# Kernel optimization log

Hardware: AMD Instinct MI355X
Metric: run time of the kernel (lower is better)

The kernel has to match this reference:

```python
import jax, jax.numpy as jnp
import numpy as np

N = 50000
E = 800000
D_IN = 128
D_HID = 128
D_OUT = 64


def setup_inputs() -> dict:
    key = jax.random.key(0)
    ks = jax.random.split(key, 9)
    x = jax.random.normal(ks[0], (N, D_IN), dtype=jnp.float32)
    edge_index = jax.random.randint(ks[1], (2, E), 0, N, dtype=jnp.int64)
    # PyG SAGEConv params: lin_l (neighbor path, with bias), lin_r (root path, no bias)
    s1 = 1.0 / np.sqrt(D_IN)
    s2 = 1.0 / np.sqrt(D_HID)
    return {
        "x": x,
        "edge_index": edge_index,
        "W1l": jax.random.uniform(ks[2], (D_IN, D_HID), jnp.float32, -s1, s1),
        "b1": jax.random.uniform(ks[3], (D_HID,), jnp.float32, -s1, s1),
        "W1r": jax.random.uniform(ks[4], (D_IN, D_HID), jnp.float32, -s1, s1),
        "W2l": jax.random.uniform(ks[5], (D_HID, D_OUT), jnp.float32, -s2, s2),
        "b2": jax.random.uniform(ks[6], (D_OUT,), jnp.float32, -s2, s2),
        "W2r": jax.random.uniform(ks[7], (D_HID, D_OUT), jnp.float32, -s2, s2),
    }


def _sage_conv(h, src, dst, Wl, b, Wr, n_nodes):
    # mean-aggregate source features onto target nodes
    msg = h[src]  # [E, d] gather
    summed = jax.ops.segment_sum(msg, dst, num_segments=n_nodes)
    cnt = jax.ops.segment_sum(jnp.ones((src.shape[0],), h.dtype), dst, num_segments=n_nodes)
    mean = summed / jnp.maximum(cnt, 1.0)[:, None]
    return mean @ Wl + b + h @ Wr


def reference(x, edge_index, W1l, b1, W1r, W2l, b2, W2r):
    src, dst = edge_index[0], edge_index[1]
    n = x.shape[0]
    h = jax.nn.relu(_sage_conv(x, src, dst, W1l, b1, W1r, n))
    # dropout is identity in eval mode
    return _sage_conv(h, src, dst, W2l, b2, W2r, n)
```

## Files before the change

kernel.cpp:

```cpp
#include <hip/hip_runtime.h>

#define NN   50000
#define NE   800000
#define CAP  48
#define NPG  6250
#define EPB  3125
#define SEG  576

#define BIN_BLOCKS  256
#define CVT_BLOCKS  (3125 + 128)
#define ZERO_BLOCKS 196
#define SCAT_BLOCKS 2048

typedef __attribute__((ext_vector_type(8))) short bf16x8;
typedef __attribute__((ext_vector_type(4))) float f32x4;

__device__ __forceinline__ unsigned short f2b(float f) {
    unsigned int u = __builtin_bit_cast(unsigned int, f);
    u += 0x7FFFu + ((u >> 16) & 1u);
    return (unsigned short)(u >> 16);
}
__device__ __forceinline__ float b2f_lo(unsigned int u) {
    return __builtin_bit_cast(float, u << 16);
}
__device__ __forceinline__ float b2f_hi(unsigned int u) {
    return __builtin_bit_cast(float, u & 0xFFFF0000u);
}

__global__ __launch_bounds__(256) void prep_kernel(const int* __restrict__ src,
                                                   const int* __restrict__ dst,
                                                   int* __restrict__ bcnt,
                                                   unsigned* __restrict__ stage,
                                                   const float* __restrict__ x,
                                                   const float* __restrict__ W1l,
                                                   const float* __restrict__ W1r,
                                                   const float* __restrict__ W2l,
                                                   const float* __restrict__ W2r,
                                                   unsigned short* __restrict__ xb,
                                                   unsigned short* __restrict__ Bt1,
                                                   unsigned short* __restrict__ Bt2,
                                                   int* __restrict__ cursor) {
    if (blockIdx.x < BIN_BLOCKS) {
        __shared__ int cnt[16][8];
        __shared__ int repoff[16][8];
        const int tid = threadIdx.x;
        const int b   = blockIdx.x;
        const int r   = tid >> 4;
        if (tid < 128) ((int*)cnt)[tid] = 0;
        __syncthreads();

        unsigned recs[13], metas[13];
#pragma unroll
        for (int it = 0; it < 13; ++it) {
            const int i = it * 256 + tid;
            metas[it] = 0xFFFFFFFFu;
            if (i < EPB) {
                const int e = b * EPB + i;
                const int s = src[e], d = dst[e];
                const int g = d / NPG;
                const int dloc = d - g * NPG;
                const int slot = atomicAdd(&cnt[r][g], 1);
                recs[it]  = ((unsigned)dloc << 16) | (unsigned)s;
                metas[it] = ((unsigned)r << 20) | ((unsigned)g << 16) | (unsigned)slot;
            }
        }
        __syncthreads();
        if (tid < 8) {
            int off = 0;
#pragma unroll
            for (int rr = 0; rr < 16; ++rr) { repoff[rr][tid] = off; off += cnt[rr][tid]; }
            bcnt[tid * 256 + b] = off;
        }
        __syncthreads();
#pragma unroll
        for (int it = 0; it < 13; ++it) {
            if (metas[it] != 0xFFFFFFFFu) {
                const int rr   = metas[it] >> 20;
                const int g    = (metas[it] >> 16) & 7;
                const int slot = metas[it] & 0xFFFF;
                const int pos  = repoff[rr][g] + slot;
                if (pos < SEG) stage[((g << 8) + b) * SEG + pos] = recs[it];
            }
        }
    } else if (blockIdx.x < BIN_BLOCKS + 3125) {
        int i = (blockIdx.x - BIN_BLOCKS) * 256 + threadIdx.x;
        const float4* p = reinterpret_cast<const float4*>(x) + (size_t)i * 2;
        float4 a = p[0], b = p[1];
        uint4 u;
        u.x = (unsigned)f2b(a.x) | ((unsigned)f2b(a.y) << 16);
        u.y = (unsigned)f2b(a.z) | ((unsigned)f2b(a.w) << 16);
        u.z = (unsigned)f2b(b.x) | ((unsigned)f2b(b.y) << 16);
        u.w = (unsigned)f2b(b.z) | ((unsigned)f2b(b.w) << 16);
        reinterpret_cast<uint4*>(xb)[i] = u;
    } else if (blockIdx.x < BIN_BLOCKS + CVT_BLOCKS) {
        int t = (blockIdx.x - BIN_BLOCKS - 3125) * 256 + threadIdx.x;
        if (t < 32768) {
            int c = t >> 8, k = t & 255;
            float v = (k < 128) ? W1l[k * 128 + c] : W1r[(k - 128) * 128 + c];
            Bt1[c * 256 + k] = f2b(v);
        }
        if (t < 16384) {
            int c = t >> 7, k = t & 127;
            float v = (c < 64) ? W2l[k * 64 + c] : W2r[k * 64 + (c - 64)];
            Bt2[c * 128 + k] = f2b(v);
        }
    } else {
        int i = (blockIdx.x - BIN_BLOCKS - CVT_BLOCKS) * 256 + threadIdx.x;
        if (i < NN) cursor[i] = 0;
    }
}

__global__ __launch_bounds__(256) void scatter_kernel(const int* __restrict__ bcnt,
                                                      const unsigned* __restrict__ stage,
                                                      int* __restrict__ cursor,
                                                      int* __restrict__ col) {
    const int g = blockIdx.x & 7;
    const int b = blockIdx.x >> 3;
    int cnt = bcnt[g * 256 + b];
    if (cnt > SEG) cnt = SEG;
    const unsigned* sp = stage + (size_t)((g << 8) + b) * SEG;
    const int n0 = g * NPG;
    for (int i = threadIdx.x; i < cnt; i += 256) {
        unsigned rec = sp[i];
        int d = n0 + (int)(rec >> 16);
        int p = atomicAdd(&cursor[d], 1);
        if (p < CAP) col[d * CAP + p] = (int)(rec & 0xFFFFu);
    }
}

__global__ __launch_bounds__(256) void agg_gemm12(const unsigned short* __restrict__ xb,
                                                  const int* __restrict__ cursor,
                                                  const int* __restrict__ col,
                                                  const unsigned short* __restrict__ Bt1,
                                                  const unsigned short* __restrict__ Bt2,
                                                  const float* __restrict__ b1,
                                                  const float* __restrict__ b2,
                                                  unsigned short* __restrict__ hlb,
                                                  float* __restrict__ outp) {
    constexpr int LDA = 264;
    constexpr int LDH = 136;
    __shared__ unsigned short As[64 * LDA];

    const int base = blockIdx.x * 64;
    const int tid  = threadIdx.x;
    const int l    = tid & 15;
    const int sub  = tid >> 4;

    const uint4* fp = reinterpret_cast<const uint4*>(xb);

    for (int gq = 0; gq < 4; ++gq) {
        const int r  = gq * 16 + sub;
        const int gn = base + r;
        float a0 = 0.f, a1 = 0.f, a2 = 0.f, a3 = 0.f,
              a4 = 0.f, a5 = 0.f, a6 = 0.f, a7 = 0.f;
        uint4 xrow = make_uint4(0, 0, 0, 0);
        if (gn < NN) {
            int len = cursor[gn];
            len = (len > CAP) ? CAP : len;
            const int4* cp = reinterpret_cast<const int4*>(col + gn * CAP);
            int j = 0;
            for (; j + 4 <= len; j += 4) {
                int4 c4 = cp[j >> 2];
                uint4 v0 = fp[c4.x * 16 + l];
                uint4 v1 = fp[c4.y * 16 + l];
                uint4 v2 = fp[c4.z * 16 + l];
                uint4 v3 = fp[c4.w * 16 + l];
                a0 += (b2f_lo(v0.x) + b2f_lo(v1.x)) + (b2f_lo(v2.x) + b2f_lo(v3.x));
                a1 += (b2f_hi(v0.x) + b2f_hi(v1.x)) + (b2f_hi(v2.x) + b2f_hi(v3.x));
                a2 += (b2f_lo(v0.y) + b2f_lo(v1.y)) + (b2f_lo(v2.y) + b2f_lo(v3.y));
                a3 += (b2f_hi(v0.y) + b2f_hi(v1.y)) + (b2f_hi(v2.y) + b2f_hi(v3.y));
                a4 += (b2f_lo(v0.z) + b2f_lo(v1.z)) + (b2f_lo(v2.z) + b2f_lo(v3.z));
                a5 += (b2f_hi(v0.z) + b2f_hi(v1.z)) + (b2f_hi(v2.z) + b2f_hi(v3.z));
                a6 += (b2f_lo(v0.w) + b2f_lo(v1.w)) + (b2f_lo(v2.w) + b2f_lo(v3.w));
                a7 += (b2f_hi(v0.w) + b2f_hi(v1.w)) + (b2f_hi(v2.w) + b2f_hi(v3.w));
            }
            for (; j < len; ++j) {
                uint4 v0 = fp[col[gn * CAP + j] * 16 + l];
                a0 += b2f_lo(v0.x);  a1 += b2f_hi(v0.x);
                a2 += b2f_lo(v0.y);  a3 += b2f_hi(v0.y);
                a4 += b2f_lo(v0.z);  a5 += b2f_hi(v0.z);
                a6 += b2f_lo(v0.w);  a7 += b2f_hi(v0.w);
            }
            const float inv = 1.0f / fmaxf((float)len, 1.0f);
            a0 *= inv; a1 *= inv; a2 *= inv; a3 *= inv;
            a4 *= inv; a5 *= inv; a6 *= inv; a7 *= inv;
            xrow = fp[gn * 16 + l];
        }
        uint4 u;
        u.x = (unsigned)f2b(a0) | ((unsigned)f2b(a1) << 16);
        u.y = (unsigned)f2b(a2) | ((unsigned)f2b(a3) << 16);
        u.z = (unsigned)f2b(a4) | ((unsigned)f2b(a5) << 16);
        u.w = (unsigned)f2b(a6) | ((unsigned)f2b(a7) << 16);
        *reinterpret_cast<uint4*>(&As[r * LDA + l * 8])       = u;
        *reinterpret_cast<uint4*>(&As[r * LDA + 128 + l * 8]) = xrow;
    }
    __syncthreads();

    const int wid  = tid >> 6, lane = tid & 63;
    const int lr   = lane & 15;
    const int lk   = (lane >> 4) * 8;
    const int ccol = lane & 15;
    const int ri   = (lane >> 4) * 4;

    f32x4 acc[4][2];
#pragma unroll
    for (int t = 0; t < 4; ++t) {
        acc[t][0] = (f32x4){0.f, 0.f, 0.f, 0.f};
        acc[t][1] = (f32x4){0.f, 0.f, 0.f, 0.f};
    }
    for (int ks = 0; ks < 8; ++ks) {
        const int k = ks * 32 + lk;
        bf16x8 b0 = *reinterpret_cast<const bf16x8*>(Bt1 + (size_t)(wid * 32 + lr) * 256 + k);
        bf16x8 b1 = *reinterpret_cast<const bf16x8*>(Bt1 + (size_t)(wid * 32 + 16 + lr) * 256 + k);
#pragma unroll
        for (int t = 0; t < 4; ++t) {
            bf16x8 a = *reinterpret_cast<const bf16x8*>(&As[(t * 16 + lr) * LDA + k]);
            acc[t][0] = __builtin_amdgcn_mfma_f32_16x16x32_bf16(a, b0, acc[t][0], 0, 0, 0);
            acc[t][1] = __builtin_amdgcn_mfma_f32_16x16x32_bf16(a, b1, acc[t][1], 0, 0, 0);
        }
    }
    __syncthreads();

    unsigned short* Hs = As;
#pragma unroll
    for (int t = 0; t < 4; ++t) {
#pragma unroll
        for (int f = 0; f < 2; ++f) {
            const int colg = wid * 32 + f * 16 + ccol;
            const float bv = b1[colg];
#pragma unroll
            for (int i = 0; i < 4; ++i) {
                Hs[(t * 16 + ri + i) * LDH + colg] = f2b(fmaxf(acc[t][f][i] + bv, 0.f));
            }
        }
    }
    __syncthreads();

    f32x4 acc2[4][2];
#pragma unroll
    for (int t = 0; t < 4; ++t) {
        acc2[t][0] = (f32x4){0.f, 0.f, 0.f, 0.f};
        acc2[t][1] = (f32x4){0.f, 0.f, 0.f, 0.f};
    }
    for (int ks = 0; ks < 4; ++ks) {
        const int k = ks * 32 + lk;
        bf16x8 b0 = *reinterpret_cast<const bf16x8*>(Bt2 + (size_t)(wid * 32 + lr) * 128 + k);
        bf16x8 b1 = *reinterpret_cast<const bf16x8*>(Bt2 + (size_t)(wid * 32 + 16 + lr) * 128 + k);
#pragma unroll
        for (int t = 0; t < 4; ++t) {
            bf16x8 a = *reinterpret_cast<const bf16x8*>(&Hs[(t * 16 + lr) * LDH + k]);
            acc2[t][0] = __builtin_amdgcn_mfma_f32_16x16x32_bf16(a, b0, acc2[t][0], 0, 0, 0);
            acc2[t][1] = __builtin_amdgcn_mfma_f32_16x16x32_bf16(a, b1, acc2[t][1], 0, 0, 0);
        }
    }

#pragma unroll
    for (int t = 0; t < 4; ++t) {
#pragma unroll
        for (int f = 0; f < 2; ++f) {
            const int colg = wid * 32 + f * 16 + ccol;
#pragma unroll
            for (int i = 0; i < 4; ++i) {
                const int gn = base + t * 16 + ri + i;
                if (gn < NN) {
                    float v = acc2[t][f][i];
                    if (colg < 64) hlb[(size_t)gn * 64 + colg] = f2b(v);
                    else           outp[(size_t)gn * 64 + (colg - 64)] = v + b2[colg - 64];
                }
            }
        }
    }
}

template <int DB>
__global__ __launch_bounds__(256) void agg_kernel(const unsigned short* __restrict__ feat,
                                                  const int* __restrict__ cursor,
                                                  const int* __restrict__ col,
                                                  float* outf) {
    constexpr int TPN = DB / 8;
    constexpr int NPB = 256 / TPN;
    const int n = blockIdx.x * NPB + threadIdx.x / TPN;
    const int l = threadIdx.x % TPN;
    if (n >= NN) return;
    int len = cursor[n];
    len = (len > CAP) ? CAP : len;
    float a0 = 0.f, a1 = 0.f, a2 = 0.f, a3 = 0.f, a4 = 0.f, a5 = 0.f, a6 = 0.f, a7 = 0.f;
    const uint4* fp = reinterpret_cast<const uint4*>(feat);
    const int4*  cp = reinterpret_cast<const int4*>(col + n * CAP);

    int j = 0;
    for (; j + 4 <= len; j += 4) {
        int4 c4 = cp[j >> 2];
        uint4 v0 = fp[c4.x * TPN + l];
        uint4 v1 = fp[c4.y * TPN + l];
        uint4 v2 = fp[c4.z * TPN + l];
        uint4 v3 = fp[c4.w * TPN + l];
        a0 += (b2f_lo(v0.x) + b2f_lo(v1.x)) + (b2f_lo(v2.x) + b2f_lo(v3.x));
        a1 += (b2f_hi(v0.x) + b2f_hi(v1.x)) + (b2f_hi(v2.x) + b2f_hi(v3.x));
        a2 += (b2f_lo(v0.y) + b2f_lo(v1.y)) + (b2f_lo(v2.y) + b2f_lo(v3.y));
        a3 += (b2f_hi(v0.y) + b2f_hi(v1.y)) + (b2f_hi(v2.y) + b2f_hi(v3.y));
        a4 += (b2f_lo(v0.z) + b2f_lo(v1.z)) + (b2f_lo(v2.z) + b2f_lo(v3.z));
        a5 += (b2f_hi(v0.z) + b2f_hi(v1.z)) + (b2f_hi(v2.z) + b2f_hi(v3.z));
        a6 += (b2f_lo(v0.w) + b2f_lo(v1.w)) + (b2f_lo(v2.w) + b2f_lo(v3.w));
        a7 += (b2f_hi(v0.w) + b2f_hi(v1.w)) + (b2f_hi(v2.w) + b2f_hi(v3.w));
    }
    for (; j < len; ++j) {
        uint4 v0 = fp[col[n * CAP + j] * TPN + l];
        a0 += b2f_lo(v0.x);  a1 += b2f_hi(v0.x);
        a2 += b2f_lo(v0.y);  a3 += b2f_hi(v0.y);
        a4 += b2f_lo(v0.z);  a5 += b2f_hi(v0.z);
        a6 += b2f_lo(v0.w);  a7 += b2f_hi(v0.w);
    }
    const float inv = 1.0f / fmaxf((float)len, 1.0f);
    a0 *= inv; a1 *= inv; a2 *= inv; a3 *= inv;
    a4 *= inv; a5 *= inv; a6 *= inv; a7 *= inv;
    const float4* ap = reinterpret_cast<const float4*>(outf + (size_t)n * DB) + l * 2;
    float4 b0 = ap[0], b1 = ap[1];
    float4 o0 = make_float4(a0 + b0.x, a1 + b0.y, a2 + b0.z, a3 + b0.w);
    float4 o1 = make_float4(a4 + b1.x, a5 + b1.y, a6 + b1.z, a7 + b1.w);
    float4* op = reinterpret_cast<float4*>(outf + (size_t)n * DB) + l * 2;
    op[0] = o0; op[1] = o1;
}

extern "C" void kernel_launch(void* const* d_in, const int* in_sizes, int n_in,
                              void* d_out, int out_size, void* d_ws, size_t ws_size,
                              hipStream_t stream) {
    const float* x   = (const float*)d_in[0];
    const int*   ei  = (const int*)d_in[1];
    const float* W1l = (const float*)d_in[2];
    const float* b1  = (const float*)d_in[3];
    const float* W1r = (const float*)d_in[4];
    const float* W2l = (const float*)d_in[5];
    const float* b2  = (const float*)d_in[6];
    const float* W2r = (const float*)d_in[7];

    const int* src = ei;
    const int* dst = ei + NE;

    char* ws = (char*)d_ws;
    int* cursor = (int*)ws;
    int* bcnt   = (int*)(ws + 200000);
    int* col    = (int*)(ws + 208384);
    unsigned short* xb  = (unsigned short*)(ws + 9808384);
    unsigned short* hlb = (unsigned short*)(ws + 22608384);
    unsigned*       stage = (unsigned*)(ws + 35408384);
    unsigned short* Bt1 = (unsigned short*)(ws + 48208384);
    unsigned short* Bt2 = (unsigned short*)(ws + 48273920);
    float* outp = (float*)d_out;

    prep_kernel<<<BIN_BLOCKS + CVT_BLOCKS + ZERO_BLOCKS, 256, 0, stream>>>(
        src, dst, bcnt, stage, x, W1l, W1r, W2l, W2r, xb, Bt1, Bt2, cursor);
    scatter_kernel<<<SCAT_BLOCKS, 256, 0, stream>>>(bcnt, stage, cursor, col);

    agg_gemm12<<<(NN + 63) / 64, 256, 0, stream>>>(xb, cursor, col, Bt1, Bt2,
                                                   b1, b2, hlb, outp);

    agg_kernel<64><<<(NN * 8 + 255) / 256, 256, 0, stream>>>(hlb, cursor, col, outp);
}
```

Measured before the change: 118.3 us.

## Shrink column indices to u16, unroll gathers by 8, store root path as bf16

Neighbor indices in the per-node adjacency table are stored as 16-bit values instead of 32-bit, which halves the index traffic. The gather loops in both aggregation kernels now process 8 neighbors per iteration. The second-layer root-path result is written as a bf16 intermediate instead of fp32 into the output, and the final kernel then writes the output once without a read-modify-write. The 16-bit indices rely on node ids being local within a 6250-node group, which the binning step appears to provide. The bf16 root term adds some rounding error.

```diff
diff --git a/kernel.cpp b/kernel.cpp
--- a/kernel.cpp
+++ b/kernel.cpp
@@ -13,6 +13,7 @@
 #define SCAT_BLOCKS 2048
 
 typedef __attribute__((ext_vector_type(8))) short bf16x8;
+typedef __attribute__((ext_vector_type(8))) unsigned short u16x8;
 typedef __attribute__((ext_vector_type(4))) float f32x4;
 
 __device__ __forceinline__ unsigned short f2b(float f) {
@@ -113,7 +114,7 @@
 __global__ __launch_bounds__(256) void scatter_kernel(const int* __restrict__ bcnt,
                                                       const unsigned* __restrict__ stage,
                                                       int* __restrict__ cursor,
-                                                      int* __restrict__ col) {
+                                                      unsigned short* __restrict__ col) {
     const int g = blockIdx.x & 7;
     const int b = blockIdx.x >> 3;
     int cnt = bcnt[g * 256 + b];
@@ -124,19 +125,18 @@
         unsigned rec = sp[i];
         int d = n0 + (int)(rec >> 16);
         int p = atomicAdd(&cursor[d], 1);
-        if (p < CAP) col[d * CAP + p] = (int)(rec & 0xFFFFu);
+        if (p < CAP) col[d * CAP + p] = (unsigned short)(rec & 0xFFFFu);
     }
 }
 
 __global__ __launch_bounds__(256) void agg_gemm12(const unsigned short* __restrict__ xb,
                                                   const int* __restrict__ cursor,
-                                                  const int* __restrict__ col,
+                                                  const unsigned short* __restrict__ col,
                                                   const unsigned short* __restrict__ Bt1,
                                                   const unsigned short* __restrict__ Bt2,
                                                   const float* __restrict__ b1,
-                                                  const float* __restrict__ b2,
                                                   unsigned short* __restrict__ hlb,
-                                                  float* __restrict__ outp) {
+                                                  unsigned short* __restrict__ hrb) {
     constexpr int LDA = 264;
     constexpr int LDH = 136;
     __shared__ unsigned short As[64 * LDA];
@@ -157,29 +157,41 @@
         if (gn < NN) {
             int len = cursor[gn];
             len = (len > CAP) ? CAP : len;
-            const int4* cp = reinterpret_cast<const int4*>(col + gn * CAP);
+            const unsigned short* cl = col + gn * CAP;
             int j = 0;
-            for (; j + 4 <= len; j += 4) {
-                int4 c4 = cp[j >> 2];
-                uint4 v0 = fp[c4.x * 16 + l];
-                uint4 v1 = fp[c4.y * 16 + l];
-                uint4 v2 = fp[c4.z * 16 + l];
-                uint4 v3 = fp[c4.w * 16 + l];
-                a0 += (b2f_lo(v0.x) + b2f_lo(v1.x)) + (b2f_lo(v2.x) + b2f_lo(v3.x));
-                a1 += (b2f_hi(v0.x) + b2f_hi(v1.x)) + (b2f_hi(v2.x) + b2f_hi(v3.x));
-                a2 += (b2f_lo(v0.y) + b2f_lo(v1.y)) + (b2f_lo(v2.y) + b2f_lo(v3.y));
-                a3 += (b2f_hi(v0.y) + b2f_hi(v1.y)) + (b2f_hi(v2.y) + b2f_hi(v3.y));
-                a4 += (b2f_lo(v0.z) + b2f_lo(v1.z)) + (b2f_lo(v2.z) + b2f_lo(v3.z));
-                a5 += (b2f_hi(v0.z) + b2f_hi(v1.z)) + (b2f_hi(v2.z) + b2f_hi(v3.z));
-                a6 += (b2f_lo(v0.w) + b2f_lo(v1.w)) + (b2f_lo(v2.w) + b2f_lo(v3.w));
-                a7 += (b2f_hi(v0.w) + b2f_hi(v1.w)) + (b2f_hi(v2.w) + b2f_hi(v3.w));
+            for (; j + 8 <= len; j += 8) {
+                u16x8 c8 = *reinterpret_cast<const u16x8*>(cl + j);
+                uint4 w0 = fp[(int)c8[0] * 16 + l];
+                uint4 w1 = fp[(int)c8[1] * 16 + l];
+                uint4 w2 = fp[(int)c8[2] * 16 + l];
+                uint4 w3 = fp[(int)c8[3] * 16 + l];
+                uint4 w4 = fp[(int)c8[4] * 16 + l];
+                uint4 w5 = fp[(int)c8[5] * 16 + l];
+                uint4 w6 = fp[(int)c8[6] * 16 + l];
+                uint4 w7 = fp[(int)c8[7] * 16 + l];
+                a0 += (b2f_lo(w0.x) + b2f_lo(w1.x)) + (b2f_lo(w2.x) + b2f_lo(w3.x))
+                    + (b2f_lo(w4.x) + b2f_lo(w5.x)) + (b2f_lo(w6.x) + b2f_lo(w7.x));
+                a1 += (b2f_hi(w0.x) + b2f_hi(w1.x)) + (b2f_hi(w2.x) + b2f_hi(w3.x))
+                    + (b2f_hi(w4.x) + b2f_hi(w5.x)) + (b2f_hi(w6.x) + b2f_hi(w7.x));
+                a2 += (b2f_lo(w0.y) + b2f_lo(w1.y)) + (b2f_lo(w2.y) + b2f_lo(w3.y))
+                    + (b2f_lo(w4.y) + b2f_lo(w5.y)) + (b2f_lo(w6.y) + b2f_lo(w7.y));
+                a3 += (b2f_hi(w0.y) + b2f_hi(w1.y)) + (b2f_hi(w2.y) + b2f_hi(w3.y))
+                    + (b2f_hi(w4.y) + b2f_hi(w5.y)) + (b2f_hi(w6.y) + b2f_hi(w7.y));
+                a4 += (b2f_lo(w0.z) + b2f_lo(w1.z)) + (b2f_lo(w2.z) + b2f_lo(w3.z))
+                    + (b2f_lo(w4.z) + b2f_lo(w5.z)) + (b2f_lo(w6.z) + b2f_lo(w7.z));
+                a5 += (b2f_hi(w0.z) + b2f_hi(w1.z)) + (b2f_hi(w2.z) + b2f_hi(w3.z))
+                    + (b2f_hi(w4.z) + b2f_hi(w5.z)) + (b2f_hi(w6.z) + b2f_hi(w7.z));
+                a6 += (b2f_lo(w0.w) + b2f_lo(w1.w)) + (b2f_lo(w2.w) + b2f_lo(w3.w))
+                    + (b2f_lo(w4.w) + b2f_lo(w5.w)) + (b2f_lo(w6.w) + b2f_lo(w7.w));
+                a7 += (b2f_hi(w0.w) + b2f_hi(w1.w)) + (b2f_hi(w2.w) + b2f_hi(w3.w))
+                    + (b2f_hi(w4.w) + b2f_hi(w5.w)) + (b2f_hi(w6.w) + b2f_hi(w7.w));
             }
             for (; j < len; ++j) {
-                uint4 v0 = fp[col[gn * CAP + j] * 16 + l];
-                a0 += b2f_lo(v0.x);  a1 += b2f_hi(v0.x);
-                a2 += b2f_lo(v0.y);  a3 += b2f_hi(v0.y);
-                a4 += b2f_lo(v0.z);  a5 += b2f_hi(v0.z);
-                a6 += b2f_lo(v0.w);  a7 += b2f_hi(v0.w);
+                uint4 w0 = fp[(int)cl[j] * 16 + l];
+                a0 += b2f_lo(w0.x);  a1 += b2f_hi(w0.x);
+                a2 += b2f_lo(w0.y);  a3 += b2f_hi(w0.y);
+                a4 += b2f_lo(w0.z);  a5 += b2f_hi(w0.z);
+                a6 += b2f_lo(w0.w);  a7 += b2f_hi(w0.w);
             }
             const float inv = 1.0f / fmaxf((float)len, 1.0f);
             a0 *= inv; a1 *= inv; a2 *= inv; a3 *= inv;
@@ -265,60 +277,76 @@
                 if (gn < NN) {
                     float v = acc2[t][f][i];
                     if (colg < 64) hlb[(size_t)gn * 64 + colg] = f2b(v);
-                    else           outp[(size_t)gn * 64 + (colg - 64)] = v + b2[colg - 64];
+                    else           hrb[(size_t)gn * 64 + (colg - 64)] = f2b(v);
                 }
             }
         }
     }
 }
 
-template <int DB>
-__global__ __launch_bounds__(256) void agg_kernel(const unsigned short* __restrict__ feat,
-                                                  const int* __restrict__ cursor,
-                                                  const int* __restrict__ col,
-                                                  float* outf) {
-    constexpr int TPN = DB / 8;
-    constexpr int NPB = 256 / TPN;
-    const int n = blockIdx.x * NPB + threadIdx.x / TPN;
-    const int l = threadIdx.x % TPN;
+__global__ __launch_bounds__(256) void agg2_kernel(const unsigned short* __restrict__ feat,
+                                                   const int* __restrict__ cursor,
+                                                   const unsigned short* __restrict__ col,
+                                                   const unsigned short* __restrict__ hrb,
+                                                   const float* __restrict__ b2,
+                                                   float* __restrict__ outf) {
+    const int n = blockIdx.x * 32 + (threadIdx.x >> 3);
+    const int l = threadIdx.x & 7;
     if (n >= NN) return;
     int len = cursor[n];
     len = (len > CAP) ? CAP : len;
     float a0 = 0.f, a1 = 0.f, a2 = 0.f, a3 = 0.f, a4 = 0.f, a5 = 0.f, a6 = 0.f, a7 = 0.f;
     const uint4* fp = reinterpret_cast<const uint4*>(feat);
-    const int4*  cp = reinterpret_cast<const int4*>(col + n * CAP);
+    const unsigned short* cl = col + n * CAP;
 
     int j = 0;
-    for (; j + 4 <= len; j += 4) {
-        int4 c4 = cp[j >> 2];
-        uint4 v0 = fp[c4.x * TPN + l];
-        uint4 v1 = fp[c4.y * TPN + l];
-        uint4 v2 = fp[c4.z * TPN + l];
-        uint4 v3 = fp[c4.w * TPN + l];
-        a0 += (b2f_lo(v0.x) + b2f_lo(v1.x)) + (b2f_lo(v2.x) + b2f_lo(v3.x));
-        a1 += (b2f_hi(v0.x) + b2f_hi(v1.x)) + (b2f_hi(v2.x) + b2f_hi(v3.x));
-        a2 += (b2f_lo(v0.y) + b2f_lo(v1.y)) + (b2f_lo(v2.y) + b2f_lo(v3.y));
-        a3 += (b2f_hi(v0.y) + b2f_hi(v1.y)) + (b2f_hi(v2.y) + b2f_hi(v3.y));
-        a4 += (b2f_lo(v0.z) + b2f_lo(v1.z)) + (b2f_lo(v2.z) + b2f_lo(v3.z));
-        a5 += (b2f_hi(v0.z) + b2f_hi(v1.z)) + (b2f_hi(v2.z) + b2f_hi(v3.z));
-        a6 += (b2f_lo(v0.w) + b2f_lo(v1.w)) + (b2f_lo(v2.w) + b2f_lo(v3.w));
-        a7 += (b2f_hi(v0.w) + b2f_hi(v1.w)) + (b2f_hi(v2.w) + b2f_hi(v3.w));
+    for (; j + 8 <= len; j += 8) {
+        u16x8 c8 = *reinterpret_cast<const u16x8*>(cl + j);
+        uint4 w0 = fp[(int)c8[0] * 8 + l];
+        uint4 w1 = fp[(int)c8[1] * 8 + l];
+        uint4 w2 = fp[(int)c8[2] * 8 + l];
+        uint4 w3 = fp[(int)c8[3] * 8 + l];
+        uint4 w4 = fp[(int)c8[4] * 8 + l];
+        uint4 w5 = fp[(int)c8[5] * 8 + l];
+        uint4 w6 = fp[(int)c8[6] * 8 + l];
+        uint4 w7 = fp[(int)c8[7] * 8 + l];
+        a0 += (b2f_lo(w0.x) + b2f_lo(w1.x)) + (b2f_lo(w2.x) + b2f_lo(w3.x))
+            + (b2f_lo(w4.x) + b2f_lo(w5.x)) + (b2f_lo(w6.x) + b2f_lo(w7.x));
+        a1 += (b2f_hi(w0.x) + b2f_hi(w1.x)) + (b2f_hi(w2.x) + b2f_hi(w3.x))
+            + (b2f_hi(w4.x) + b2f_hi(w5.x)) + (b2f_hi(w6.x) + b2f_hi(w7.x));
+        a2 += (b2f_lo(w0.y) + b2f_lo(w1.y)) + (b2f_lo(w2.y) + b2f_lo(w3.y))
+            + (b2f_lo(w4.y) + b2f_lo(w5.y)) + (b2f_lo(w6.y) + b2f_lo(w7.y));
+        a3 += (b2f_hi(w0.y) + b2f_hi(w1.y)) + (b2f_hi(w2.y) + b2f_hi(w3.y))
+            + (b2f_hi(w4.y) + b2f_hi(w5.y)) + (b2f_hi(w6.y) + b2f_hi(w7.y));
+        a4 += (b2f_lo(w0.z) + b2f_lo(w1.z)) + (b2f_lo(w2.z) + b2f_lo(w3.z))
+            + (b2f_lo(w4.z) + b2f_lo(w5.z)) + (b2f_lo(w6.z) + b2f_lo(w7.z));
+        a5 += (b2f_hi(w0.z) + b2f_hi(w1.z)) + (b2f_hi(w2.z) + b2f_hi(w3.z))
+            + (b2f_hi(w4.z) + b2f_hi(w5.z)) + (b2f_hi(w6.z) + b2f_hi(w7.z));
+        a6 += (b2f_lo(w0.w) + b2f_lo(w1.w)) + (b2f_lo(w2.w) + b2f_lo(w3.w))
+            + (b2f_lo(w4.w) + b2f_lo(w5.w)) + (b2f_lo(w6.w) + b2f_lo(w7.w));
+        a7 += (b2f_hi(w0.w) + b2f_hi(w1.w)) + (b2f_hi(w2.w) + b2f_hi(w3.w))
+            + (b2f_hi(w4.w) + b2f_hi(w5.w)) + (b2f_hi(w6.w) + b2f_hi(w7.w));
     }
     for (; j < len; ++j) {
-        uint4 v0 = fp[col[n * CAP + j] * TPN + l];
-        a0 += b2f_lo(v0.x);  a1 += b2f_hi(v0.x);
-        a2 += b2f_lo(v0.y);  a3 += b2f_hi(v0.y);
-        a4 += b2f_lo(v0.z);  a5 += b2f_hi(v0.z);
-        a6 += b2f_lo(v0.w);  a7 += b2f_hi(v0.w);
+        uint4 w0 = fp[(int)cl[j] * 8 + l];
+        a0 += b2f_lo(w0.x);  a1 += b2f_hi(w0.x);
+        a2 += b2f_lo(w0.y);  a3 += b2f_hi(w0.y);
+        a4 += b2f_lo(w0.z);  a5 += b2f_hi(w0.z);
+        a6 += b2f_lo(w0.w);  a7 += b2f_hi(w0.w);
     }
     const float inv = 1.0f / fmaxf((float)len, 1.0f);
-    a0 *= inv; a1 *= inv; a2 *= inv; a3 *= inv;
-    a4 *= inv; a5 *= inv; a6 *= inv; a7 *= inv;
-    const float4* ap = reinterpret_cast<const float4*>(outf + (size_t)n * DB) + l * 2;
-    float4 b0 = ap[0], b1 = ap[1];
-    float4 o0 = make_float4(a0 + b0.x, a1 + b0.y, a2 + b0.z, a3 + b0.w);
-    float4 o1 = make_float4(a4 + b1.x, a5 + b1.y, a6 + b1.z, a7 + b1.w);
-    float4* op = reinterpret_cast<float4*>(outf + (size_t)n * DB) + l * 2;
+    uint4 hv = reinterpret_cast<const uint4*>(hrb)[(size_t)n * 8 + l];
+    const float4* bp = reinterpret_cast<const float4*>(b2 + l * 8);
+    float4 bv0 = bp[0], bv1 = bp[1];
+    float4 o0 = make_float4(a0 * inv + b2f_lo(hv.x) + bv0.x,
+                            a1 * inv + b2f_hi(hv.x) + bv0.y,
+                            a2 * inv + b2f_lo(hv.y) + bv0.z,
+                            a3 * inv + b2f_hi(hv.y) + bv0.w);
+    float4 o1 = make_float4(a4 * inv + b2f_lo(hv.z) + bv1.x,
+                            a5 * inv + b2f_hi(hv.z) + bv1.y,
+                            a6 * inv + b2f_lo(hv.w) + bv1.z,
+                            a7 * inv + b2f_hi(hv.w) + bv1.w);
+    float4* op = reinterpret_cast<float4*>(outf + (size_t)n * 64) + l * 2;
     op[0] = o0; op[1] = o1;
 }
 
@@ -340,9 +368,10 @@
     char* ws = (char*)d_ws;
     int* cursor = (int*)ws;
     int* bcnt   = (int*)(ws + 200000);
-    int* col    = (int*)(ws + 208384);
+    unsigned short* col = (unsigned short*)(ws + 208384);
     unsigned short* xb  = (unsigned short*)(ws + 9808384);
     unsigned short* hlb = (unsigned short*)(ws + 22608384);
+    unsigned short* hrb = (unsigned short*)(ws + 29008384);
     unsigned*       stage = (unsigned*)(ws + 35408384);
     unsigned short* Bt1 = (unsigned short*)(ws + 48208384);
     unsigned short* Bt2 = (unsigned short*)(ws + 48273920);
@@ -353,7 +382,7 @@
     scatter_kernel<<<SCAT_BLOCKS, 256, 0, stream>>>(bcnt, stage, cursor, col);
 
     agg_gemm12<<<(NN + 63) / 64, 256, 0, stream>>>(xb, cursor, col, Bt1, Bt2,
-                                                   b1, b2, hlb, outp);
-
-    agg_kernel<64><<<(NN * 8 + 255) / 256, 256, 0, stream>>>(hlb, cursor, col, outp);
-}
+                                                   b1, hlb, hrb);
+
+    agg2_kernel<<<(NN + 31) / 32, 256, 0, stream>>>(hlb, cursor, col, hrb, b2, outp);
+}
```

New measurement: 140.8 us. +19.1%, slower.

## Store adjacency as u16 and keep root-path output as bf16 until final aggregation

Applied to the files above, without the earlier changes.

Neighbor index lists are stored as 16-bit values instead of 32-bit, halving adjacency storage and the index reads in both aggregation passes. The second-layer root-path product is written as bf16 to a separate scratch buffer rather than as fp32 into the output. The final aggregation kernel then adds this term and the bias, replacing an fp32 read-modify-write of the output with a bf16 read plus one write. This trades extra bf16 rounding on the root-path term for less memory traffic.

```diff
diff --git a/kernel.cpp b/kernel.cpp
--- a/kernel.cpp
+++ b/kernel.cpp
@@ -13,6 +13,7 @@
 #define SCAT_BLOCKS 2048
 
 typedef __attribute__((ext_vector_type(8))) short bf16x8;
+typedef __attribute__((ext_vector_type(4))) unsigned short u16x4;
 typedef __attribute__((ext_vector_type(4))) float f32x4;
 
 __device__ __forceinline__ unsigned short f2b(float f) {
@@ -113,7 +114,7 @@
 __global__ __launch_bounds__(256) void scatter_kernel(const int* __restrict__ bcnt,
                                                       const unsigned* __restrict__ stage,
                                                       int* __restrict__ cursor,
-                                                      int* __restrict__ col) {
+                                                      unsigned short* __restrict__ col) {
     const int g = blockIdx.x & 7;
     const int b = blockIdx.x >> 3;
     int cnt = bcnt[g * 256 + b];
@@ -124,19 +125,18 @@
         unsigned rec = sp[i];
         int d = n0 + (int)(rec >> 16);
         int p = atomicAdd(&cursor[d], 1);
-        if (p < CAP) col[d * CAP + p] = (int)(rec & 0xFFFFu);
+        if (p < CAP) col[d * CAP + p] = (unsigned short)(rec & 0xFFFFu);
     }
 }
 
 __global__ __launch_bounds__(256) void agg_gemm12(const unsigned short* __restrict__ xb,
                                                   const int* __restrict__ cursor,
-                                                  const int* __restrict__ col,
+                                                  const unsigned short* __restrict__ col,
                                                   const unsigned short* __restrict__ Bt1,
                                                   const unsigned short* __restrict__ Bt2,
                                                   const float* __restrict__ b1,
-                                                  const float* __restrict__ b2,
                                                   unsigned short* __restrict__ hlb,
-                                                  float* __restrict__ outp) {
+                                                  unsigned short* __restrict__ hrb) {
     constexpr int LDA = 264;
     constexpr int LDH = 136;
     __shared__ unsigned short As[64 * LDA];
@@ -157,14 +157,14 @@
         if (gn < NN) {
             int len = cursor[gn];
             len = (len > CAP) ? CAP : len;
-            const int4* cp = reinterpret_cast<const int4*>(col + gn * CAP);
+            const unsigned short* cl = col + gn * CAP;
             int j = 0;
             for (; j + 4 <= len; j += 4) {
-                int4 c4 = cp[j >> 2];
-                uint4 v0 = fp[c4.x * 16 + l];
-                uint4 v1 = fp[c4.y * 16 + l];
-                uint4 v2 = fp[c4.z * 16 + l];
-                uint4 v3 = fp[c4.w * 16 + l];
+                u16x4 c4 = *reinterpret_cast<const u16x4*>(cl + j);
+                uint4 v0 = fp[(int)c4[0] * 16 + l];
+                uint4 v1 = fp[(int)c4[1] * 16 + l];
+                uint4 v2 = fp[(int)c4[2] * 16 + l];
+                uint4 v3 = fp[(int)c4[3] * 16 + l];
                 a0 += (b2f_lo(v0.x) + b2f_lo(v1.x)) + (b2f_lo(v2.x) + b2f_lo(v3.x));
                 a1 += (b2f_hi(v0.x) + b2f_hi(v1.x)) + (b2f_hi(v2.x) + b2f_hi(v3.x));
                 a2 += (b2f_lo(v0.y) + b2f_lo(v1.y)) + (b2f_lo(v2.y) + b2f_lo(v3.y));
@@ -175,7 +175,7 @@
                 a7 += (b2f_hi(v0.w) + b2f_hi(v1.w)) + (b2f_hi(v2.w) + b2f_hi(v3.w));
             }
             for (; j < len; ++j) {
-                uint4 v0 = fp[col[gn * CAP + j] * 16 + l];
+                uint4 v0 = fp[(int)cl[j] * 16 + l];
                 a0 += b2f_lo(v0.x);  a1 += b2f_hi(v0.x);
                 a2 += b2f_lo(v0.y);  a3 += b2f_hi(v0.y);
                 a4 += b2f_lo(v0.z);  a5 += b2f_hi(v0.z);
@@ -265,36 +265,35 @@
                 if (gn < NN) {
                     float v = acc2[t][f][i];
                     if (colg < 64) hlb[(size_t)gn * 64 + colg] = f2b(v);
-                    else           outp[(size_t)gn * 64 + (colg - 64)] = v + b2[colg - 64];
+                    else           hrb[(size_t)gn * 64 + (colg - 64)] = f2b(v);
                 }
             }
         }
     }
 }
 
-template <int DB>
-__global__ __launch_bounds__(256) void agg_kernel(const unsigned short* __restrict__ feat,
-                                                  const int* __restrict__ cursor,
-                                                  const int* __restrict__ col,
-                                                  float* outf) {
-    constexpr int TPN = DB / 8;
-    constexpr int NPB = 256 / TPN;
-    const int n = blockIdx.x * NPB + threadIdx.x / TPN;
-    const int l = threadIdx.x % TPN;
+__global__ __launch_bounds__(256) void agg2_kernel(const unsigned short* __restrict__ feat,
+                                                   const int* __restrict__ cursor,
+                                                   const unsigned short* __restrict__ col,
+                                                   const unsigned short* __restrict__ hrb,
+                                                   const float* __restrict__ b2,
+                                                   float* __restrict__ outf) {
+    const int n = blockIdx.x * 32 + (threadIdx.x >> 3);
+    const int l = threadIdx.x & 7;
     if (n >= NN) return;
     int len = cursor[n];
     len = (len > CAP) ? CAP : len;
     float a0 = 0.f, a1 = 0.f, a2 = 0.f, a3 = 0.f, a4 = 0.f, a5 = 0.f, a6 = 0.f, a7 = 0.f;
     const uint4* fp = reinterpret_cast<const uint4*>(feat);
-    const int4*  cp = reinterpret_cast<const int4*>(col + n * CAP);
+    const unsigned short* cl = col + n * CAP;
 
     int j = 0;
     for (; j + 4 <= len; j += 4) {
-        int4 c4 = cp[j >> 2];
-        uint4 v0 = fp[c4.x * TPN + l];
-        uint4 v1 = fp[c4.y * TPN + l];
-        uint4 v2 = fp[c4.z * TPN + l];
-        uint4 v3 = fp[c4.w * TPN + l];
+        u16x4 c4 = *reinterpret_cast<const u16x4*>(cl + j);
+        uint4 v0 = fp[(int)c4[0] * 8 + l];
+        uint4 v1 = fp[(int)c4[1] * 8 + l];
+        uint4 v2 = fp[(int)c4[2] * 8 + l];
+        uint4 v3 = fp[(int)c4[3] * 8 + l];
         a0 += (b2f_lo(v0.x) + b2f_lo(v1.x)) + (b2f_lo(v2.x) + b2f_lo(v3.x));
         a1 += (b2f_hi(v0.x) + b2f_hi(v1.x)) + (b2f_hi(v2.x) + b2f_hi(v3.x));
         a2 += (b2f_lo(v0.y) + b2f_lo(v1.y)) + (b2f_lo(v2.y) + b2f_lo(v3.y));
@@ -305,20 +304,25 @@
         a7 += (b2f_hi(v0.w) + b2f_hi(v1.w)) + (b2f_hi(v2.w) + b2f_hi(v3.w));
     }
     for (; j < len; ++j) {
-        uint4 v0 = fp[col[n * CAP + j] * TPN + l];
+        uint4 v0 = fp[(int)cl[j] * 8 + l];
         a0 += b2f_lo(v0.x);  a1 += b2f_hi(v0.x);
         a2 += b2f_lo(v0.y);  a3 += b2f_hi(v0.y);
         a4 += b2f_lo(v0.z);  a5 += b2f_hi(v0.z);
         a6 += b2f_lo(v0.w);  a7 += b2f_hi(v0.w);
     }
     const float inv = 1.0f / fmaxf((float)len, 1.0f);
-    a0 *= inv; a1 *= inv; a2 *= inv; a3 *= inv;
-    a4 *= inv; a5 *= inv; a6 *= inv; a7 *= inv;
-    const float4* ap = reinterpret_cast<const float4*>(outf + (size_t)n * DB) + l * 2;
-    float4 b0 = ap[0], b1 = ap[1];
-    float4 o0 = make_float4(a0 + b0.x, a1 + b0.y, a2 + b0.z, a3 + b0.w);
-    float4 o1 = make_float4(a4 + b1.x, a5 + b1.y, a6 + b1.z, a7 + b1.w);
-    float4* op = reinterpret_cast<float4*>(outf + (size_t)n * DB) + l * 2;
+    uint4 hv = reinterpret_cast<const uint4*>(hrb)[(size_t)n * 8 + l];
+    const float4* bp = reinterpret_cast<const float4*>(b2 + l * 8);
+    float4 bv0 = bp[0], bv1 = bp[1];
+    float4 o0 = make_float4(a0 * inv + b2f_lo(hv.x) + bv0.x,
+                            a1 * inv + b2f_hi(hv.x) + bv0.y,
+                            a2 * inv + b2f_lo(hv.y) + bv0.z,
+                            a3 * inv + b2f_hi(hv.y) + bv0.w);
+    float4 o1 = make_float4(a4 * inv + b2f_lo(hv.z) + bv1.x,
+                            a5 * inv + b2f_hi(hv.z) + bv1.y,
+                            a6 * inv + b2f_lo(hv.w) + bv1.z,
+                            a7 * inv + b2f_hi(hv.w) + bv1.w);
+    float4* op = reinterpret_cast<float4*>(outf + (size_t)n * 64) + l * 2;
     op[0] = o0; op[1] = o1;
 }
 
@@ -340,9 +344,10 @@
     char* ws = (char*)d_ws;
     int* cursor = (int*)ws;
     int* bcnt   = (int*)(ws + 200000);
-    int* col    = (int*)(ws + 208384);
+    unsigned short* col = (unsigned short*)(ws + 208384);
     unsigned short* xb  = (unsigned short*)(ws + 9808384);
     unsigned short* hlb = (unsigned short*)(ws + 22608384);
+    unsigned short* hrb = (unsigned short*)(ws + 29008384);
     unsigned*       stage = (unsigned*)(ws + 35408384);
     unsigned short* Bt1 = (unsigned short*)(ws + 48208384);
     unsigned short* Bt2 = (unsigned short*)(ws + 48273920);
@@ -353,7 +358,7 @@
     scatter_kernel<<<SCAT_BLOCKS, 256, 0, stream>>>(bcnt, stage, cursor, col);
 
     agg_gemm12<<<(NN + 63) / 64, 256, 0, stream>>>(xb, cursor, col, Bt1, Bt2,
-                                                   b1, b2, hlb, outp);
-
-    agg_kernel<64><<<(NN * 8 + 255) / 256, 256, 0, stream>>>(hlb, cursor, col, outp);
-}
+                                                   b1, hlb, hrb);
+
+    agg2_kernel<<<(NN + 31) / 32, 256, 0, stream>>>(hlb, cursor, col, hrb, b2, outp);
+}
```

Result: faster. 115.0 us (-2.7%).
